# Kernel optimization log

Measured on AMD Instinct MI355X. Metric: run time of the kernel, lower is better.

## Reference

```python
import jax, jax.numpy as jnp
import numpy as np


def _unfold3x3(x):
    # Matches torch F.unfold(kernel=(3,3), padding=1): output (B, C*9, H*W)
    # with feature layout (c, kh, kw) -- channel-major, kernel-position minor.
    B, C, H, W = x.shape
    xp = jnp.pad(x, ((0, 0), (0, 0), (1, 1), (1, 1)))
    patches = jnp.stack(
        [xp[:, :, i:i + H, j:j + W] for i in range(3) for j in range(3)],
        axis=2,
    )  # (B, C, 9, H, W)
    return patches.reshape(B, C * 9, H * W)


def setup_inputs() -> dict:
    key = jax.random.key(0)
    x = jax.random.normal(key, (4, 64, 64, 64), dtype=jnp.float32)
    return {"x": x}


def reference(x):
    B, C, H, W = x.shape
    HW = H * W
    xu = _unfold3x3(x)  # (B, C*9, HW)
    # torch F.normalize(dim=2): L2-normalize each (b, feature) row over spatial dim
    norm = jnp.maximum(jnp.linalg.norm(xu, axis=2, keepdims=True), 1e-12)
    xu = xu / norm
    # dense correlation over all positions: (B, HW, HW)
    R = jnp.einsum('bdn,bdm->bnm', xu, xu)
    _, idx = jax.lax.top_k(R, 3)  # idx: (B, HW, 3)
    # gather the top-3 neighbor patch columns; fixed k=3 loop (structural, not data dim)
    stacks = []
    for k in range(3):
        idx_k = idx[:, :, k][:, None, :]                    # (B, 1, HW)
        g = jnp.take_along_axis(xu, idx_k, axis=2)          # (B, C*9, HW)
        # torch: permute(0,2,1).reshape(B, HW, -1, C) -> (B, HW, 9, C)
        stacks.append(jnp.transpose(g, (0, 2, 1)).reshape(B, HW, 9, C))
    K = jnp.concatenate(stacks, axis=2)                     # (B, HW, 27, C)
    Q = jnp.transpose(x.reshape(B, C, HW), (0, 2, 1))       # (B, HW, C)
    scores = jnp.einsum('bnc,bnkc->bnk', Q, K) / jnp.sqrt(jnp.float32(C))
    w = jax.nn.softmax(scores, axis=2)                      # (B, HW, 27)
    return jnp.einsum('bnk,bnkc->bnc', w, K)                # (B, HW, C)
```

## Files before the change

kernel.cpp:

```cpp
#include <hip/hip_runtime.h>
#include <cstdint>

typedef short short8 __attribute__((ext_vector_type(8)));
typedef float f32x16 __attribute__((ext_vector_type(16)));

#define NB 4
#define NN 4096
#define ND 576
#define BIGI 0x7FFFFFFF
#define NSLICE 4

#define INVN_OFF 9437184
#define CANDV_OFF 9439488
#define CANDI_OFF 9636096

#define MFMA __builtin_amdgcn_mfma_f32_32x32x16_bf16

__device__ __forceinline__ unsigned short f2bf(float f) {
    unsigned u = __float_as_uint(f);
    u += 0x7FFFu + ((u >> 16) & 1u);
    return (unsigned short)(u >> 16);
}

__device__ __forceinline__ void insert_cmp(float v, int m,
    float& v0, int& i0, float& v1, int& i1, float& v2, int& i2) {
    bool beat2 = (v > v2) || (v == v2 && m < i2);
    if (beat2) {
        bool beat1 = (v > v1) || (v == v1 && m < i1);
        if (beat1) {
            v2 = v1; i2 = i1;
            bool beat0 = (v > v0) || (v == v0 && m < i0);
            if (beat0) { v1 = v0; i1 = i0; v0 = v; i0 = m; }
            else       { v1 = v;  i1 = m; }
        } else { v2 = v; i2 = m; }
    }
}

__global__ __launch_bounds__(64) void norm_kernel(const float* __restrict__ x,
                                                  float* __restrict__ ws) {
    const int bc = blockIdx.x;
    const int lane = threadIdx.x;
    const float* xp = x + ((size_t)bc << 12);
    float colsum = 0.f, v0 = 0.f, v63 = 0.f;
    for (int h = 0; h < 64; ++h) {
        const float val = xp[(h << 6) + lane];
        const float sq = val * val;
        colsum += sq;
        if (h == 0)  v0 = sq;
        if (h == 63) v63 = sq;
    }
    float total = colsum, row0 = v0, row63 = v63;
    #pragma unroll
    for (int o = 32; o > 0; o >>= 1) {
        total += __shfl_xor(total, o);
        row0  += __shfl_xor(row0, o);
        row63 += __shfl_xor(row63, o);
    }
    const float col0  = __shfl(colsum, 0);
    const float col63 = __shfl(colsum, 63);
    const float c00 = __shfl(v0, 0),  c0e = __shfl(v0, 63);
    const float ce0 = __shfl(v63, 0), cee = __shfl(v63, 63);
    if (lane < 9) {
        const int dh = lane / 3 - 1, dw = lane % 3 - 1;
        float S = total;
        if (dh == 1)  S -= row0;
        if (dh == -1) S -= row63;
        if (dw == 1)  S -= col0;
        if (dw == -1) S -= col63;
        if (dh == 1  && dw == 1)  S += c00;
        if (dh == 1  && dw == -1) S += c0e;
        if (dh == -1 && dw == 1)  S += ce0;
        if (dh == -1 && dw == -1) S += cee;
        float nrm = fmaxf(sqrtf(S), 1e-12f);
        ws[INVN_OFF + bc * 9 + lane] = 1.0f / nrm;
    }
}

__global__ __launch_bounds__(256) void mat_kernel(const float* __restrict__ x,
                                                  float* __restrict__ ws) {
    const int bi = blockIdx.x;
    const int b = bi / 576;
    const int rem = bi - b * 576;
    const int nt = rem / 18;
    const int kc = rem - nt * 18;
    unsigned short* AH = (unsigned short*)ws;
    unsigned short* AL = AH + 9437184;
    const float* invn = ws + INVN_OFF + b * 576;
    const int tid = threadIdx.x;
    #pragma unroll
    for (int hf2 = 0; hf2 < 2; ++hf2) {
        const int c = tid + hf2 * 256;
        const int row = c >> 2, k0 = (c & 3) * 8;
        const int n = nt * 128 + row;
        const int h = n >> 6, wc = n & 63;
        union { unsigned short us[8]; float4 f4; } uh, ul;
        #pragma unroll
        for (int j = 0; j < 8; ++j) {
            const int d = kc * 32 + k0 + j;
            const int ch = d / 9;
            const int p = d - ch * 9;
            const int r = h + p / 3 - 1, s2 = wc + p % 3 - 1;
            float val = 0.f;
            if ((unsigned)r < 64u && (unsigned)s2 < 64u)
                val = x[((size_t)(b * 64 + ch) << 12) + (r << 6) + s2];
            val *= invn[d];
            const unsigned short hb = f2bf(val);
            const float hfv = __uint_as_float(((unsigned)hb) << 16);
            const unsigned short lb = f2bf(val - hfv);
            uh.us[j] = hb; ul.us[j] = lb;
        }
        ((float4*)AH)[(size_t)bi * 512 + c] = uh.f4;
        ((float4*)AL)[(size_t)bi * 512 + c] = ul.f4;
    }
}

__device__ __forceinline__ void stage_region(unsigned short* dst,
                                             const unsigned short* gsrc, int tid) {
    const float4* g = (const float4*)gsrc;
    #pragma unroll
    for (int i = 0; i < 2; ++i) {
        const int c = tid + i * 256;
        const float4 v = g[c];
        float2* d = (float2*)(dst + (c >> 2) * 36 + (c & 3) * 8);
        d[0] = make_float2(v.x, v.y);
        d[1] = make_float2(v.z, v.w);
    }
}

__device__ __forceinline__ short8 ldfrag(const unsigned short* p) {
    union { short8 s8; float2 f2[2]; } u;
    const float2* q = (const float2*)p;
    u.f2[0] = q[0]; u.f2[1] = q[1];
    return u.s8;
}

__global__ void __launch_bounds__(256, 2) gram_kernel(float* ws) {
    __shared__ unsigned short sm[27648];
    const int bx = blockIdx.x;
    const int b = bx >> 7;
    const int nt = (bx >> 2) & 31;
    const int s = bx & 3;
    const int tid = threadIdx.x;
    const int w = tid >> 6, lane = tid & 63;
    const int l31 = lane & 31, kh2 = lane >> 5;

    const unsigned short* AH = (const unsigned short*)ws;
    const unsigned short* AL = AH + 9437184;

    const int AnH = 0, AnL = 4608, AmH = 9216, AmL = 18432;
    const int afr = (w * 64 + l31) * 36 + kh2 * 8;
    const int bfr = l31 * 36 + kh2 * 8;

    const int nRegBase = (b * 32 + nt) * 18;

    float t0v[4], t1v[4], t2v[4];
    int   t0i[4], t1i[4], t2i[4];
    #pragma unroll
    for (int i = 0; i < 4; ++i) {
        t0v[i] = t1v[i] = t2v[i] = -INFINITY;
        t0i[i] = t1i[i] = t2i[i] = BIGI;
    }

    for (int mt = 0; mt < 4; ++mt) {
        const int mm0 = (s * 4 + mt) * 2;
        const int mReg0 = (b * 32 + mm0) * 18;
        const int mReg1 = mReg0 + 18;

        f32x16 acc[2][4];
        #pragma unroll
        for (int mi = 0; mi < 2; ++mi)
            #pragma unroll
            for (int ni = 0; ni < 4; ++ni)
                #pragma unroll
                for (int e = 0; e < 16; ++e) acc[mi][ni][e] = 0.f;

        for (int kc = 0; kc < 18; ++kc) {
            __syncthreads();
            stage_region(sm + AnH,        AH + (size_t)(nRegBase + kc) * 4096, tid);
            stage_region(sm + AnL,        AL + (size_t)(nRegBase + kc) * 4096, tid);
            stage_region(sm + AmH,        AH + (size_t)(mReg0 + kc) * 4096, tid);
            stage_region(sm + AmH + 4608, AH + (size_t)(mReg1 + kc) * 4096, tid);
            stage_region(sm + AmL,        AL + (size_t)(mReg0 + kc) * 4096, tid);
            stage_region(sm + AmL + 4608, AL + (size_t)(mReg1 + kc) * 4096, tid);
            __syncthreads();
            #pragma unroll
            for (int h = 0; h < 2; ++h) {
                short8 amh[2], aml[2];
                #pragma unroll
                for (int mi = 0; mi < 2; ++mi) {
                    amh[mi] = ldfrag(sm + AmH + afr + mi * 1152 + h * 16);
                    aml[mi] = ldfrag(sm + AmL + afr + mi * 1152 + h * 16);
                }
                #pragma unroll
                for (int ni = 0; ni < 4; ++ni) {
                    const short8 bh = ldfrag(sm + AnH + bfr + ni * 1152 + h * 16);
                    const short8 bl = ldfrag(sm + AnL + bfr + ni * 1152 + h * 16);
                    #pragma unroll
                    for (int mi = 0; mi < 2; ++mi) {
                        acc[mi][ni] = MFMA(amh[mi], bh, acc[mi][ni], 0, 0, 0);
                        acc[mi][ni] = MFMA(amh[mi], bl, acc[mi][ni], 0, 0, 0);
                        acc[mi][ni] = MFMA(aml[mi], bh, acc[mi][ni], 0, 0, 0);
                    }
                }
            }
        }
        const int mbase = (s * 4 + mt) * 256 + w * 64 + kh2 * 4;
        #pragma unroll
        for (int ni = 0; ni < 4; ++ni)
            #pragma unroll
            for (int mi = 0; mi < 2; ++mi)
                #pragma unroll
                for (int v = 0; v < 16; ++v) {
                    const int m = mbase + mi * 32 + (v & 3) + 8 * (v >> 2);
                    insert_cmp(acc[mi][ni][v], m,
                               t0v[ni], t0i[ni], t1v[ni], t1i[ni], t2v[ni], t2i[ni]);
                }
    }

    #pragma unroll
    for (int ni = 0; ni < 4; ++ni) {
        const float pv0 = __shfl_xor(t0v[ni], 32);
        const float pv1 = __shfl_xor(t1v[ni], 32);
        const float pv2 = __shfl_xor(t2v[ni], 32);
        const int pi0 = __shfl_xor(t0i[ni], 32);
        const int pi1 = __shfl_xor(t1i[ni], 32);
        const int pi2 = __shfl_xor(t2i[ni], 32);
        insert_cmp(pv0, pi0, t0v[ni], t0i[ni], t1v[ni], t1i[ni], t2v[ni], t2i[ni]);
        insert_cmp(pv1, pi1, t0v[ni], t0i[ni], t1v[ni], t1i[ni], t2v[ni], t2i[ni]);
        insert_cmp(pv2, pi2, t0v[ni], t0i[ni], t1v[ni], t1i[ni], t2v[ni], t2i[ni]);
    }
    __syncthreads();
    float* cv = (float*)sm;
    int*   ci = (int*)sm + 1536;
    if (kh2 == 0) {
        #pragma unroll
        for (int ni = 0; ni < 4; ++ni) {
            const int base = ((w * 4 + ni) * 32 + l31) * 3;
            cv[base] = t0v[ni]; cv[base + 1] = t1v[ni]; cv[base + 2] = t2v[ni];
            ci[base] = t0i[ni]; ci[base + 1] = t1i[ni]; ci[base + 2] = t2i[ni];
        }
    }
    __syncthreads();
    if (tid < 128) {
        const int ni = tid >> 5, l = tid & 31;
        float v0 = -INFINITY, v1 = -INFINITY, v2 = -INFINITY;
        int i0 = BIGI, i1 = BIGI, i2 = BIGI;
        #pragma unroll
        for (int w2 = 0; w2 < 4; ++w2) {
            const int base = ((w2 * 4 + ni) * 32 + l) * 3;
            #pragma unroll
            for (int j = 0; j < 3; ++j)
                insert_cmp(cv[base + j], ci[base + j], v0, i0, v1, i1, v2, i2);
        }
        const int n_local = ni * 32 + l;
        const size_t o = ((size_t)(b * NSLICE + s) * NN + nt * 128 + n_local) * 3;
        ws[CANDV_OFF + o] = v0; ws[CANDV_OFF + o + 1] = v1; ws[CANDV_OFF + o + 2] = v2;
        int* wi = (int*)ws;
        wi[CANDI_OFF + o] = i0; wi[CANDI_OFF + o + 1] = i1; wi[CANDI_OFF + o + 2] = i2;
    }
}

__global__ __launch_bounds__(256) void attn_kernel(const float* __restrict__ x,
                                                   const float* __restrict__ ws,
                                                   float* __restrict__ out) {
    const int wid = threadIdx.x >> 6;
    const int lane = threadIdx.x & 63;
    const int gw = blockIdx.x * 4 + wid;
    const int b = gw >> 12;
    const int n = gw & 4095;

    float v0 = -INFINITY, v1 = -INFINITY, v2 = -INFINITY;
    int i0 = BIGI, i1 = BIGI, i2 = BIGI;
    const int* wi = (const int*)ws;
    #pragma unroll
    for (int s = 0; s < NSLICE; ++s) {
        const size_t o = ((size_t)(b * NSLICE + s) * NN + n) * 3;
        #pragma unroll
        for (int j = 0; j < 3; ++j)
            insert_cmp(ws[CANDV_OFF + o + j], wi[CANDI_OFF + o + j], v0, i0, v1, i1, v2, i2);
    }
    const int idx3[3] = {i0, i1, i2};

    int cc[9], dhh[9], dww[9];
    float inr[9];
    #pragma unroll
    for (int a = 0; a < 9; ++a) {
        const int d = a * 64 + lane;
        const int c = d / 9;
        const int p = d - c * 9;
        cc[a] = c; dhh[a] = p / 3 - 1; dww[a] = p - (p / 3) * 3 - 1;
        inr[a] = ws[INVN_OFF + b * ND + d];
    }
    const float q = x[((size_t)(b * 64 + lane) << 12) + n];

    float rv[27], sc[27];
    #pragma unroll
    for (int k = 0; k < 3; ++k) {
        const int m = idx3[k];
        const int hm = m >> 6, wm = m & 63;
        #pragma unroll
        for (int a = 0; a < 9; ++a) {
            const int r = hm + dhh[a], s2 = wm + dww[a];
            float val = 0.f;
            if ((unsigned)r < 64u && (unsigned)s2 < 64u)
                val = x[((size_t)(b * 64 + cc[a]) << 12) + (r << 6) + s2];
            const float rr = val * inr[a];
            rv[k * 9 + a] = rr;
            float t = q * rr;
            #pragma unroll
            for (int o2 = 32; o2 > 0; o2 >>= 1) t += __shfl_xor(t, o2);
            sc[k * 9 + a] = t * 0.125f;
        }
    }
    float mx = -INFINITY;
    #pragma unroll
    for (int u = 0; u < 27; ++u) mx = fmaxf(mx, sc[u]);
    float sum = 0.f;
    #pragma unroll
    for (int u = 0; u < 27; ++u) { const float e = expf(sc[u] - mx); sc[u] = e; sum += e; }
    const float inv = 1.0f / sum;
    float o = 0.f;
    #pragma unroll
    for (int u = 0; u < 27; ++u) o += sc[u] * rv[u];
    out[((size_t)gw << 6) + lane] = o * inv;
}

extern "C" void kernel_launch(void* const* d_in, const int* in_sizes, int n_in,
                              void* d_out, int out_size, void* d_ws, size_t ws_size,
                              hipStream_t stream) {
    (void)in_sizes; (void)n_in; (void)out_size; (void)ws_size;
    const float* x = (const float*)d_in[0];
    float* ws = (float*)d_ws;
    float* out = (float*)d_out;

    hipLaunchKernelGGL(norm_kernel, dim3(NB * 64), dim3(64), 0, stream, x, ws);
    hipLaunchKernelGGL(mat_kernel, dim3(2304), dim3(256), 0, stream, x, ws);
    hipLaunchKernelGGL(gram_kernel, dim3(512), dim3(256), 0, stream, ws);
    hipLaunchKernelGGL(attn_kernel, dim3(4096), dim3(256), 0, stream, x, ws, out);
}
```

Measured before the change: 693.0 us.

## Stage Gram tiles via direct global-to-LDS loads with XOR-swizzled layout

Result: faster. 662.6 us (-4.4%).

```diff
diff --git a/kernel.cpp b/kernel.cpp
--- a/kernel.cpp
+++ b/kernel.cpp
@@ -20,6 +20,12 @@
     unsigned u = __float_as_uint(f);
     u += 0x7FFFu + ((u >> 16) & 1u);
     return (unsigned short)(u >> 16);
+}
+
+__device__ __forceinline__ void gload_lds16(const void* g, void* l) {
+    __builtin_amdgcn_global_load_lds(
+        (const __attribute__((address_space(1))) void*)g,
+        (__attribute__((address_space(3))) void*)l, 16, 0, 0);
 }
 
 __device__ __forceinline__ void insert_cmp(float v, int m,
@@ -89,8 +95,10 @@
     const int tid = threadIdx.x;
     #pragma unroll
     for (int hf2 = 0; hf2 < 2; ++hf2) {
-        const int c = tid + hf2 * 256;
-        const int row = c >> 2, k0 = (c & 3) * 8;
+        const int g = tid + hf2 * 256;
+        const int row = g >> 2, cp = g & 3;
+        const int c = cp ^ ((row >> 1) & 3);
+        const int k0 = c * 8;
         const int n = nt * 128 + row;
         const int h = n >> 6, wc = n & 63;
         union { unsigned short us[8]; float4 f4; } uh, ul;
@@ -109,33 +117,19 @@
             const unsigned short lb = f2bf(val - hfv);
             uh.us[j] = hb; ul.us[j] = lb;
         }
-        ((float4*)AH)[(size_t)bi * 512 + c] = uh.f4;
-        ((float4*)AL)[(size_t)bi * 512 + c] = ul.f4;
-    }
-}
-
-__device__ __forceinline__ void stage_region(unsigned short* dst,
-                                             const unsigned short* gsrc, int tid) {
-    const float4* g = (const float4*)gsrc;
-    #pragma unroll
-    for (int i = 0; i < 2; ++i) {
-        const int c = tid + i * 256;
-        const float4 v = g[c];
-        float2* d = (float2*)(dst + (c >> 2) * 36 + (c & 3) * 8);
-        d[0] = make_float2(v.x, v.y);
-        d[1] = make_float2(v.z, v.w);
-    }
-}
-
-__device__ __forceinline__ short8 ldfrag(const unsigned short* p) {
-    union { short8 s8; float2 f2[2]; } u;
-    const float2* q = (const float2*)p;
-    u.f2[0] = q[0]; u.f2[1] = q[1];
+        ((float4*)AH)[(size_t)bi * 512 + g] = uh.f4;
+        ((float4*)AL)[(size_t)bi * 512 + g] = ul.f4;
+    }
+}
+
+__device__ __forceinline__ short8 ldfrag(const short* p) {
+    union { short8 s8; float4 f4; } u;
+    u.f4 = *(const float4*)p;
     return u.s8;
 }
 
 __global__ void __launch_bounds__(256, 2) gram_kernel(float* ws) {
-    __shared__ unsigned short sm[27648];
+    __shared__ short sm[24576];
     const int bx = blockIdx.x;
     const int b = bx >> 7;
     const int nt = (bx >> 2) & 31;
@@ -147,10 +141,7 @@
     const unsigned short* AH = (const unsigned short*)ws;
     const unsigned short* AL = AH + 9437184;
 
-    const int AnH = 0, AnL = 4608, AmH = 9216, AmL = 18432;
-    const int afr = (w * 64 + l31) * 36 + kh2 * 8;
-    const int bfr = l31 * 36 + kh2 * 8;
-
+    const int AnH = 0, AnL = 4096, AmH = 8192, AmL = 16384;
     const int nRegBase = (b * 32 + nt) * 18;
 
     float t0v[4], t1v[4], t2v[4];
@@ -160,6 +151,27 @@
         t0v[i] = t1v[i] = t2v[i] = -INFINITY;
         t0i[i] = t1i[i] = t2i[i] = BIGI;
     }
+
+    int aoff[2][2][2];
+    int boff[4][2];
+    #pragma unroll
+    for (int mi = 0; mi < 2; ++mi)
+        #pragma unroll
+        for (int h = 0; h < 2; ++h) {
+            const int row = w * 64 + mi * 32 + l31;
+            const int rl = row & 127, rt = row >> 7;
+            const int c = kh2 + 2 * h;
+            aoff[mi][h][0] = rt * 4096 + rl * 32 + (c ^ ((rl >> 1) & 3)) * 8;
+            aoff[mi][h][1] = 0;
+        }
+    #pragma unroll
+    for (int ni = 0; ni < 4; ++ni)
+        #pragma unroll
+        for (int h = 0; h < 2; ++h) {
+            const int row = ni * 32 + l31;
+            const int c = kh2 + 2 * h;
+            boff[ni][h] = row * 32 + (c ^ ((row >> 1) & 3)) * 8;
+        }
 
     for (int mt = 0; mt < 4; ++mt) {
         const int mm0 = (s * 4 + mt) * 2;
@@ -176,25 +188,42 @@
 
         for (int kc = 0; kc < 18; ++kc) {
             __syncthreads();
-            stage_region(sm + AnH,        AH + (size_t)(nRegBase + kc) * 4096, tid);
-            stage_region(sm + AnL,        AL + (size_t)(nRegBase + kc) * 4096, tid);
-            stage_region(sm + AmH,        AH + (size_t)(mReg0 + kc) * 4096, tid);
-            stage_region(sm + AmH + 4608, AH + (size_t)(mReg1 + kc) * 4096, tid);
-            stage_region(sm + AmL,        AL + (size_t)(mReg0 + kc) * 4096, tid);
-            stage_region(sm + AmL + 4608, AL + (size_t)(mReg1 + kc) * 4096, tid);
+            {
+                const int i0 = w * 2, i1 = w * 2 + 1;
+                const int lo0 = i0 * 512, lo1 = i1 * 512;
+                const int go0 = lo0 + lane * 8, go1 = lo1 + lane * 8;
+                const unsigned short* gAnH = AH + (size_t)(nRegBase + kc) * 4096;
+                const unsigned short* gAnL = AL + (size_t)(nRegBase + kc) * 4096;
+                const unsigned short* gM0H = AH + (size_t)(mReg0 + kc) * 4096;
+                const unsigned short* gM1H = AH + (size_t)(mReg1 + kc) * 4096;
+                const unsigned short* gM0L = AL + (size_t)(mReg0 + kc) * 4096;
+                const unsigned short* gM1L = AL + (size_t)(mReg1 + kc) * 4096;
+                gload_lds16(gAnH + go0, sm + AnH + lo0);
+                gload_lds16(gAnH + go1, sm + AnH + lo1);
+                gload_lds16(gAnL + go0, sm + AnL + lo0);
+                gload_lds16(gAnL + go1, sm + AnL + lo1);
+                gload_lds16(gM0H + go0, sm + AmH + lo0);
+                gload_lds16(gM0H + go1, sm + AmH + lo1);
+                gload_lds16(gM1H + go0, sm + AmH + 4096 + lo0);
+                gload_lds16(gM1H + go1, sm + AmH + 4096 + lo1);
+                gload_lds16(gM0L + go0, sm + AmL + lo0);
+                gload_lds16(gM0L + go1, sm + AmL + lo1);
+                gload_lds16(gM1L + go0, sm + AmL + 4096 + lo0);
+                gload_lds16(gM1L + go1, sm + AmL + 4096 + lo1);
+            }
             __syncthreads();
             #pragma unroll
             for (int h = 0; h < 2; ++h) {
                 short8 amh[2], aml[2];
                 #pragma unroll
                 for (int mi = 0; mi < 2; ++mi) {
-                    amh[mi] = ldfrag(sm + AmH + afr + mi * 1152 + h * 16);
-                    aml[mi] = ldfrag(sm + AmL + afr + mi * 1152 + h * 16);
+                    amh[mi] = ldfrag(sm + AmH + aoff[mi][h][0]);
+                    aml[mi] = ldfrag(sm + AmL + aoff[mi][h][0]);
                 }
                 #pragma unroll
                 for (int ni = 0; ni < 4; ++ni) {
-                    const short8 bh = ldfrag(sm + AnH + bfr + ni * 1152 + h * 16);
-                    const short8 bl = ldfrag(sm + AnL + bfr + ni * 1152 + h * 16);
+                    const short8 bh = ldfrag(sm + AnH + boff[ni][h]);
+                    const short8 bl = ldfrag(sm + AnL + boff[ni][h]);
                     #pragma unroll
                     for (int mi = 0; mi < 2; ++mi) {
                         acc[mi][ni] = MFMA(amh[mi], bh, acc[mi][ni], 0, 0, 0);
```
